# Kernel tuning notes

Measured on AMD Instinct MI355X. Metric: run time of the kernel, lower is better.

## Reference

```python
import jax, jax.numpy as jnp
import numpy as np

K = 5  # kernel_size per dim
# 2^dim = 4 active degree-1 B-spline products per edge (dim=2)
BITS = jnp.array([[0, 0], [1, 0], [0, 1], [1, 1]], dtype=jnp.int32)  # [S,2]


def spline_basis(edge_attr):
    """Open B-spline basis, degree=1, dim=2, kernel_size=5 per dim.
    Returns basis weights [E,S] and flattened kernel indices [E,S]."""
    v = edge_attr * (K - 1)                 # scale pseudo-coords to knot grid
    i0 = jnp.floor(v)
    f = v - i0                              # fractional part, [E,2]
    # per-dim linear weights: f for bit=1, (1-f) for bit=0
    w = jnp.where(BITS[None] == 1, f[:, None, :], 1.0 - f[:, None, :])  # [E,S,2]
    basis = w[..., 0] * w[..., 1]           # [E,S]
    idx = jnp.minimum(i0.astype(jnp.int32)[:, None, :] + BITS[None], K - 1)  # [E,S,2]
    kidx = idx[..., 0] + K * idx[..., 1]    # flatten 2D kernel index -> [0,25)
    return basis, kidx


def spline_conv(x, src, dst, basis, kidx, W, root, bias, n):
    # transform-then-gather: y[n,k,:] = x[n] @ W[k]
    y = jnp.einsum('ni,kio->nko', x, W)                 # [N,25,out]
    g = y[src[:, None], kidx]                           # gather [E,S,out]
    msg = jnp.einsum('es,eso->eo', basis, g)            # weighted sum over S
    agg = jax.ops.segment_sum(msg, dst, num_segments=n)  # scatter-add to targets
    return agg + x @ root + bias                        # root weight + bias


def setup_inputs() -> dict:
    key = jax.random.key(0)
    ks = jax.random.split(key, 8)
    N, E, IN, H, OUT = 50000, 400000, 32, 64, 64
    x = jax.random.normal(ks[0], (N, IN), jnp.float32)
    edge_index = jax.random.randint(ks[1], (2, E), 0, N, dtype=jnp.int32)
    edge_attr = jax.random.uniform(ks[2], (E, 2), jnp.float32)

    def glorot(k, shape):
        fan = shape[-2] + shape[-1]
        return jax.random.normal(k, shape, jnp.float32) * jnp.sqrt(2.0 / fan)

    W1 = glorot(ks[3], (K * K, IN, H));  root1 = glorot(ks[4], (IN, H));  b1 = jnp.zeros((H,), jnp.float32)
    W2 = glorot(ks[5], (K * K, H, OUT)); root2 = glorot(ks[6], (H, OUT)); b2 = jnp.zeros((OUT,), jnp.float32)
    fc_w = glorot(ks[7], (OUT, 3));      fc_b = jnp.zeros((3,), jnp.float32)
    return dict(x=x, edge_index=edge_index, edge_attr=edge_attr,
                W1=W1, root1=root1, b1=b1, W2=W2, root2=root2, b2=b2,
                fc_w=fc_w, fc_b=fc_b)


def reference(x, edge_index, edge_attr, W1, root1, b1, W2, root2, b2, fc_w, fc_b):
    # eval-mode forward (dropout is identity at inference)
    n = x.shape[0]
    src, dst = edge_index[0], edge_index[1]
    basis, kidx = spline_basis(edge_attr)
    h = jax.nn.relu(spline_conv(x, src, dst, basis, kidx, W1, root1, b1, n))
    h = jax.nn.relu(spline_conv(h, src, dst, basis, kidx, W2, root2, b2, n))
    return h @ fc_w + fc_b
```

## Files before the change

kernel.cpp:

```cpp
#include <hip/hip_runtime.h>
#include <stdint.h>

typedef __attribute__((ext_vector_type(8))) short short8;
typedef __attribute__((ext_vector_type(4))) float f32x4;
typedef __attribute__((ext_vector_type(4))) unsigned short ushort4v;

__device__ __forceinline__ unsigned short f2bf(float f) {
    unsigned int u = __float_as_uint(f);
    u = (u + 0x7FFFu + ((u >> 16) & 1u)) >> 16;
    return (unsigned short)u;
}
__device__ __forceinline__ float bf2f(unsigned short h) {
    return __uint_as_float(((unsigned int)h) << 16);
}
__device__ __forceinline__ int cell_of(float ax, float ay) {
    int c0 = (int)floorf(ax * 4.f); c0 = min(max(c0, 0), 3);
    int c1 = (int)floorf(ay * 4.f); c1 = min(max(c1, 0), 3);
    return c0 + 4 * c1;
}

__global__ __launch_bounds__(256) void zero_kernel(int* __restrict__ p, int n) {
    int t = blockIdx.x * 256 + threadIdx.x;
    if (t < n) p[t] = 0;
}

template<int KIN>
__device__ __forceinline__ void pack_cell_elem(const float* __restrict__ W,
                                               unsigned short* __restrict__ pkc, int u) {
    constexpr int KCH = KIN / 8;
    if (u >= 16 * 4 * KCH * 512) return;
    int low9 = u & 511;
    int grp  = u >> 9;
    int kc = grp % KCH; grp /= KCH;
    int c  = grp & 3;
    int cell = grp >> 2;
    int lane = low9 >> 3, j = low9 & 7;
    int k = kc * 32 + (lane >> 4) * 8 + j;
    int t = k / KIN, i = k % KIN;
    int k0 = (cell & 3) + (t & 1);   if (k0 > 4) k0 = 4;
    int k1 = (cell >> 2) + (t >> 1); if (k1 > 4) k1 = 4;
    float val = W[((size_t)(k0 + 5 * k1) * KIN + i) * 64 + (c * 16 + (lane & 15))];
    pkc[u] = f2bf(val);
}

template<int KIN>
__device__ __forceinline__ void pack_root_elem(const float* __restrict__ root,
                                               unsigned short* __restrict__ pkr, int u) {
    constexpr int KCHr = KIN / 32;
    if (u >= 4 * KCHr * 512) return;
    int low9 = u & 511;
    int grp  = u >> 9;
    int lane = low9 >> 3, j = low9 & 7;
    int kc = grp % KCHr, c = grp / KCHr;
    int k = kc * 32 + (lane >> 4) * 8 + j;
    int o = c * 16 + (lane & 15);
    float v = root[(size_t)k * 64 + o];
    unsigned short h = f2bf(v);
    pkr[(size_t)(grp * 2) * 512 + low9]     = h;
    pkr[(size_t)(grp * 2 + 1) * 512 + low9] = f2bf(v - bf2f(h));
}

__global__ __launch_bounds__(256) void prep_kernel(
    const float* __restrict__ attr, const int* __restrict__ dst,
    int* __restrict__ hist, int* __restrict__ dhist, int E,
    const float* __restrict__ W1, const float* __restrict__ W2,
    const float* __restrict__ root1, const float* __restrict__ root2,
    unsigned short* __restrict__ pkc1, unsigned short* __restrict__ pkc2,
    unsigned short* __restrict__ pkr1, unsigned short* __restrict__ pkr2,
    const float* __restrict__ x, unsigned short* __restrict__ xb, int n4,
    int EB)
{
    __shared__ int wcnt[4][16];
    int b = blockIdx.x;
    if (b < EB) {
        int e = b * 256 + threadIdx.x;
        int lane = threadIdx.x & 63, wave = threadIdx.x >> 6;
        int cell = -1;
        if (e < E) {
            float2 a = reinterpret_cast<const float2*>(attr)[e];
            cell = cell_of(a.x, a.y);
            atomicAdd(&dhist[dst[e]], 1);
        }
        #pragma unroll
        for (int c = 0; c < 16; c++) {
            unsigned long long m = __ballot(cell == c);
            if (lane == 0) wcnt[wave][c] = __popcll(m);
        }
        __syncthreads();
        if (threadIdx.x < 16) {
            int c = threadIdx.x;
            int tot = wcnt[0][c] + wcnt[1][c] + wcnt[2][c] + wcnt[3][c];
            if (tot) atomicAdd(&hist[c], tot);
        }
        return;
    }
    b -= EB;
    if (b < 512)  { pack_cell_elem<32>(W1, pkc1, b * 256 + threadIdx.x); return; }
    b -= 512;
    if (b < 1024) { pack_cell_elem<64>(W2, pkc2, b * 256 + threadIdx.x); return; }
    b -= 1024;
    if (b < 8)    { pack_root_elem<32>(root1, pkr1, b * 256 + threadIdx.x); return; }
    b -= 8;
    if (b < 16)   { pack_root_elem<64>(root2, pkr2, b * 256 + threadIdx.x); return; }
    b -= 16;
    {
        int t = b * 256 + threadIdx.x;
        if (t < n4) {
            float4 v = reinterpret_cast<const float4*>(x)[t];
            ushort4v o = { f2bf(v.x), f2bf(v.y), f2bf(v.z), f2bf(v.w) };
            reinterpret_cast<ushort4v*>(xb)[t] = o;
        }
    }
}

__global__ __launch_bounds__(1024) void scanA_kernel(const int* __restrict__ dhist,
                                                     int* __restrict__ nof,
                                                     int* __restrict__ bsum, int Np1) {
    __shared__ int wsum[16];
    int tid = threadIdx.x, lane = tid & 63, w = tid >> 6;
    int i = blockIdx.x * 1024 + tid;
    int v = (i < Np1) ? dhist[i] : 0;
    int s = v;
    #pragma unroll
    for (int off = 1; off < 64; off <<= 1) {
        int t = __shfl_up(s, off);
        if (lane >= off) s += t;
    }
    if (lane == 63) wsum[w] = s;
    __syncthreads();
    if (tid == 0) {
        int a = 0;
        #pragma unroll
        for (int k = 0; k < 16; k++) { int t = wsum[k]; wsum[k] = a; a += t; }
        bsum[blockIdx.x] = a;
    }
    __syncthreads();
    if (i < Np1) nof[i] = wsum[w] + s - v;
}

__global__ void scan_small_kernel(const int* __restrict__ hist, int* __restrict__ off_e,
                                  int* __restrict__ off_b, int* __restrict__ cursor,
                                  const int* __restrict__ bsum, int* __restrict__ bbase, int NB) {
    if (threadIdx.x == 0 && blockIdx.x == 0) {
        int se = 0, sb = 0;
        for (int c = 0; c < 16; c++) {
            off_e[c] = se; off_b[c] = sb; cursor[c] = se;
            se += hist[c]; sb += (hist[c] + 63) >> 6;
        }
        off_e[16] = se; off_b[16] = sb;
        int a = 0;
        for (int bks = 0; bks < NB; bks++) { int t = bsum[bks]; bbase[bks] = a; a += t; }
    }
}

__global__ __launch_bounds__(256) void scatter_kernel(const float* __restrict__ attr,
                                                      const int* __restrict__ src,
                                                      const int* __restrict__ dst,
                                                      const int* __restrict__ nof,
                                                      const int* __restrict__ bbase,
                                                      int4* __restrict__ emeta,
                                                      int* __restrict__ cursor,
                                                      int* __restrict__ dhist, int E) {
    __shared__ int wcnt[4][16];
    __shared__ int wbase[4][16];
    int e = blockIdx.x * 256 + threadIdx.x;
    int lane = threadIdx.x & 63, wave = threadIdx.x >> 6;
    int cell = -1;
    float2 a = {0.f, 0.f};
    int mp = 0, sv = 0;
    if (e < E) {
        a = reinterpret_cast<const float2*>(attr)[e];
        cell = cell_of(a.x, a.y);
        int d = dst[e];
        int rank = atomicSub(&dhist[d], 1) - 1;
        mp = nof[d] + bbase[d >> 10] + rank;
        sv = src[e];
    }
    int myrank = 0;
    #pragma unroll
    for (int c = 0; c < 16; c++) {
        unsigned long long m = __ballot(cell == c);
        if (cell == c) myrank = __popcll(m & ((1ull << lane) - 1ull));
        if (lane == 0) wcnt[wave][c] = __popcll(m);
    }
    __syncthreads();
    if (threadIdx.x < 16) {
        int c = threadIdx.x;
        int t0 = wcnt[0][c], t1 = wcnt[1][c], t2 = wcnt[2][c], t3 = wcnt[3][c];
        int tot = t0 + t1 + t2 + t3;
        int g = tot ? atomicAdd(&cursor[c], tot) : 0;
        wbase[0][c] = g;
        wbase[1][c] = g + t0;
        wbase[2][c] = g + t0 + t1;
        wbase[3][c] = g + t0 + t1 + t2;
    }
    __syncthreads();
    if (e < E) {
        int slot = wbase[wave][cell] + myrank;
        emeta[slot] = make_int4(sv, mp, __float_as_int(a.x), __float_as_int(a.y));
    }
}

template<int KIN>
__global__ __launch_bounds__(256) void layer_kernel(
    const unsigned short* __restrict__ Xb,
    const unsigned short* __restrict__ pkr, float* __restrict__ rt,
    const float* __restrict__ bias, int N, int RG,
    const unsigned short* __restrict__ pkc, unsigned short* __restrict__ msg,
    const int4* __restrict__ emeta,
    const int* __restrict__ off_e, const int* __restrict__ off_b)
{
    constexpr int KCHr = KIN / 32;
    constexpr int KCH  = 4 * KCHr;

    const int lane = threadIdx.x & 63;
    const int wave = threadIdx.x >> 6;
    const int lrow = lane & 15, lch = lane >> 4;

    if (blockIdx.x < RG) {
        const int mbase = blockIdx.x * 64 + wave * 16;
        short8 afrag[KCHr];
        {
            int row = mbase + lrow;
            if (row > N - 1) row = N - 1;
            const unsigned short* ap = Xb + (size_t)row * KIN + lch * 8;
            #pragma unroll
            for (int kc = 0; kc < KCHr; kc++)
                afrag[kc] = *reinterpret_cast<const short8*>(ap + kc * 32);
        }
        f32x4 acc[4];
        #pragma unroll
        for (int c = 0; c < 4; c++) acc[c] = (f32x4){0.f, 0.f, 0.f, 0.f};
        #pragma unroll
        for (int c = 0; c < 4; c++) {
            #pragma unroll
            for (int kc = 0; kc < KCHr; kc++) {
                short8 bh = *reinterpret_cast<const short8*>(pkr + ((size_t)(c * KCHr + kc) * 2    ) * 512 + lane * 8);
                short8 bl = *reinterpret_cast<const short8*>(pkr + ((size_t)(c * KCHr + kc) * 2 + 1) * 512 + lane * 8);
                acc[c] = __builtin_amdgcn_mfma_f32_16x16x32_bf16(afrag[kc], bh, acc[c], 0, 0, 0);
                acc[c] = __builtin_amdgcn_mfma_f32_16x16x32_bf16(afrag[kc], bl, acc[c], 0, 0, 0);
            }
        }
        #pragma unroll
        for (int c = 0; c < 4; c++) {
            int o = c * 16 + lrow;
            float bv = bias[o];
            #pragma unroll
            for (int r = 0; r < 4; r++) {
                int m = mbase + lch * 4 + r;
                if (m < N) rt[(size_t)m * 64 + o] = acc[c][r] + bv;
            }
        }
        return;
    }

    const int b = blockIdx.x - RG;
    if (b >= off_b[16]) return;
    int cell = 0;
    #pragma unroll
    for (int c = 1; c < 16; c++) cell += (b >= off_b[c]);
    const int tile = b - off_b[cell];

    const int ebeg = off_e[cell];
    const int eend = off_e[cell + 1];
    const int eslot = ebeg + (tile * 4 + wave) * 16 + lrow;
    const bool valid = eslot < eend;

    const int4 em = emeta[valid ? eslot : ebeg];
    const int s = em.x;
    const int mp = valid ? em.y : -1;
    const float ax = __int_as_float(em.z);
    const float ay = __int_as_float(em.w);

    const float f0 = ax * 4.f - (float)(cell & 3);
    const float f1 = ay * 4.f - (float)(cell >> 2);
    float w[4] = { (1.f - f0) * (1.f - f1), f0 * (1.f - f1),
                   (1.f - f0) * f1,         f0 * f1 };

    short8 xfrag[KCHr];
    {
        const unsigned short* xp = Xb + (size_t)s * KIN + lch * 8;
        #pragma unroll
        for (int kcr = 0; kcr < KCHr; kcr++)
            xfrag[kcr] = *reinterpret_cast<const short8*>(xp + kcr * 32);
    }

    float wr[4][4];
    int pv[4];
    #pragma unroll
    for (int r = 0; r < 4; r++) {
        int er = lch * 4 + r;
        #pragma unroll
        for (int t = 0; t < 4; t++) wr[t][r] = __shfl(w[t], er);
        pv[r] = __shfl(mp, er);
    }

    const unsigned short* Bp = pkc + (size_t)cell * (4 * KCH * 512) + lane * 8;

    #pragma unroll
    for (int ch = 0; ch < 2; ch++) {
        f32x4 accT[4][2];
        #pragma unroll
        for (int t = 0; t < 4; t++)
            #pragma unroll
            for (int c2 = 0; c2 < 2; c2++)
                accT[t][c2] = (f32x4){0.f, 0.f, 0.f, 0.f};

        #pragma unroll
        for (int t = 0; t < 4; t++) {
            #pragma unroll
            for (int kcr = 0; kcr < KCHr; kcr++) {
                #pragma unroll
                for (int c2 = 0; c2 < 2; c2++) {
                    int c = ch * 2 + c2;
                    short8 bf = *reinterpret_cast<const short8*>(
                        Bp + (size_t)((c * KCH) + (t * KCHr + kcr)) * 512);
                    accT[t][c2] = __builtin_amdgcn_mfma_f32_16x16x32_bf16(xfrag[kcr], bf, accT[t][c2], 0, 0, 0);
                }
            }
        }

        #pragma unroll
        for (int c2 = 0; c2 < 2; c2++) {
            const int o = (ch * 2 + c2) * 16 + lrow;
            #pragma unroll
            for (int r = 0; r < 4; r++) {
                if (pv[r] >= 0) {
                    float m = wr[0][r] * accT[0][c2][r] + wr[1][r] * accT[1][c2][r]
                            + wr[2][r] * accT[2][c2][r] + wr[3][r] * accT[3][c2][r];
                    msg[(size_t)pv[r] * 64 + o] = f2bf(m);
                }
            }
        }
    }
}

template<int MODE>
__global__ __launch_bounds__(256) void segsum_kernel(
    const unsigned short* __restrict__ msg, const float* __restrict__ rt,
    const int* __restrict__ nof, const int* __restrict__ bbase,
    unsigned short* __restrict__ hout,
    const float* __restrict__ fcw, const float* __restrict__ fcb,
    float* __restrict__ out, int N)
{
    int n = blockIdx.x * 4 + (threadIdx.x >> 6);
    if (n >= N) return;
    int lane = threadIdx.x & 63;
    float acc = rt[(size_t)n * 64 + lane];
    int jb = nof[n]     + bbase[n >> 10];
    int je = nof[n + 1] + bbase[(n + 1) >> 10];
    int j = jb;
    for (; j + 3 < je; j += 4) {
        float a0 = bf2f(msg[(size_t)(j + 0) * 64 + lane]);
        float a1 = bf2f(msg[(size_t)(j + 1) * 64 + lane]);
        float a2 = bf2f(msg[(size_t)(j + 2) * 64 + lane]);
        float a3 = bf2f(msg[(size_t)(j + 3) * 64 + lane]);
        acc += a0; acc += a1; acc += a2; acc += a3;
    }
    for (; j < je; j++) acc += bf2f(msg[(size_t)j * 64 + lane]);
    acc = fmaxf(acc, 0.f);
    if (MODE == 0) {
        hout[(size_t)n * 64 + lane] = f2bf(acc);
    } else {
        float p0 = acc * fcw[lane * 3 + 0];
        float p1 = acc * fcw[lane * 3 + 1];
        float p2 = acc * fcw[lane * 3 + 2];
        #pragma unroll
        for (int off = 32; off; off >>= 1) {
            p0 += __shfl_xor(p0, off);
            p1 += __shfl_xor(p1, off);
            p2 += __shfl_xor(p2, off);
        }
        if (lane == 0) {
            out[(size_t)n * 3 + 0] = p0 + fcb[0];
            out[(size_t)n * 3 + 1] = p1 + fcb[1];
            out[(size_t)n * 3 + 2] = p2 + fcb[2];
        }
    }
}

extern "C" void kernel_launch(void* const* d_in, const int* in_sizes, int n_in,
                              void* d_out, int out_size, void* d_ws, size_t ws_size,
                              hipStream_t stream)
{
    const float* x     = (const float*)d_in[0];
    const int*   ei    = (const int*)  d_in[1];
    const float* attr  = (const float*)d_in[2];
    const float* W1    = (const float*)d_in[3];
    const float* root1 = (const float*)d_in[4];
    const float* b1    = (const float*)d_in[5];
    const float* W2    = (const float*)d_in[6];
    const float* root2 = (const float*)d_in[7];
    const float* b2    = (const float*)d_in[8];
    const float* fcw   = (const float*)d_in[9];
    const float* fcb   = (const float*)d_in[10];

    const int N = in_sizes[0] / 32;
    const int E = in_sizes[1] / 2;
    const int* srcp = ei;
    const int* dstp = ei + E;

    char* wsp = (char*)d_ws;
    auto alloc = [&](size_t bytes) -> char* {
        char* p = wsp;
        wsp += (bytes + 255) & ~(size_t)255;
        return p;
    };
    const int NB = (N + 1 + 1023) / 1024;

    float*          rt       = (float*)alloc((size_t)N * 64 * 4);
    unsigned short* xb       = (unsigned short*)alloc((size_t)N * 32 * 2);
    unsigned short* h1b      = (unsigned short*)alloc((size_t)N * 64 * 2);
    unsigned short* pkr1     = (unsigned short*)alloc((size_t)4 * 1 * 2 * 512 * 2);
    unsigned short* pkr2     = (unsigned short*)alloc((size_t)4 * 2 * 2 * 512 * 2);
    unsigned short* pkc1     = (unsigned short*)alloc((size_t)16 * 4 * 4 * 512 * 2);
    unsigned short* pkc2     = (unsigned short*)alloc((size_t)16 * 4 * 8 * 512 * 2);
    int4*           emeta    = (int4*)alloc((size_t)E * 16);
    int*            nof      = (int*)alloc((size_t)(N + 1) * 4);
    int*            bsum     = (int*)alloc((size_t)NB * 4);
    int*            bbase    = (int*)alloc((size_t)NB * 4);
    int*            off_e    = (int*)alloc(17 * 4);
    int*            off_b    = (int*)alloc(17 * 4);
    int*            cursor   = (int*)alloc(16 * 4);
    int*            zbase    = (int*)alloc((size_t)(16 + N + 1) * 4);
    int*            hist     = zbase;
    int*            dhist    = zbase + 16;
    unsigned short* msg      = (unsigned short*)alloc((size_t)E * 64 * 2);

    const int ZN = 16 + N + 1;
    zero_kernel<<<(ZN + 255) / 256, 256, 0, stream>>>(zbase, ZN);

    const int EB = (E + 255) / 256;
    const int CB = (N * 8 + 255) / 256;
    const int prep_grid = EB + 512 + 1024 + 8 + 16 + CB;

    prep_kernel<<<prep_grid, 256, 0, stream>>>(attr, dstp, hist, dhist, E,
                                               W1, W2, root1, root2,
                                               pkc1, pkc2, pkr1, pkr2,
                                               x, xb, N * 8, EB);
    scanA_kernel<<<NB, 1024, 0, stream>>>(dhist, nof, bsum, N + 1);
    scan_small_kernel<<<1, 64, 0, stream>>>(hist, off_e, off_b, cursor, bsum, bbase, NB);
    scatter_kernel<<<EB, 256, 0, stream>>>(attr, srcp, dstp, nof, bbase, emeta, cursor, dhist, E);

    const int RG = (N + 63) / 64;
    const int lgrid = RG + (E + 63) / 64 + 16;
    const int sgrid = (N + 3) / 4;

    layer_kernel<32><<<lgrid, 256, 0, stream>>>(xb, pkr1, rt, b1, N, RG,
                                                pkc1, msg, emeta, off_e, off_b);
    segsum_kernel<0><<<sgrid, 256, 0, stream>>>(msg, rt, nof, bbase, h1b, fcw, fcb, (float*)d_out, N);

    layer_kernel<64><<<lgrid, 256, 0, stream>>>(h1b, pkr2, rt, b2, N, RG,
                                                pkc2, msg, emeta, off_e, off_b);
    segsum_kernel<1><<<sgrid, 256, 0, stream>>>(msg, rt, nof, bbase, nullptr, fcw, fcb, (float*)d_out, N);
}
```

Measured before the change: 192.3 us.

## Stage per-cell spline weights in LDS and process 512-edge chunks per block

```diff
diff --git a/kernel.cpp b/kernel.cpp
--- a/kernel.cpp
+++ b/kernel.cpp
@@ -4,6 +4,8 @@
 typedef __attribute__((ext_vector_type(8))) short short8;
 typedef __attribute__((ext_vector_type(4))) float f32x4;
 typedef __attribute__((ext_vector_type(4))) unsigned short ushort4v;
+
+#define CHUNK 512
 
 __device__ __forceinline__ unsigned short f2bf(float f) {
     unsigned int u = __float_as_uint(f);
@@ -145,7 +147,7 @@
         int se = 0, sb = 0;
         for (int c = 0; c < 16; c++) {
             off_e[c] = se; off_b[c] = sb; cursor[c] = se;
-            se += hist[c]; sb += (hist[c] + 63) >> 6;
+            se += hist[c]; sb += (hist[c] + CHUNK - 1) / CHUNK;
         }
         off_e[16] = se; off_b[16] = sb;
         int a = 0;
@@ -212,6 +214,7 @@
 {
     constexpr int KCHr = KIN / 32;
     constexpr int KCH  = 4 * KCHr;
+    __shared__ unsigned short Blds[4 * KCH * 512];
 
     const int lane = threadIdx.x & 63;
     const int wave = threadIdx.x >> 6;
@@ -259,76 +262,90 @@
     int cell = 0;
     #pragma unroll
     for (int c = 1; c < 16; c++) cell += (b >= off_b[c]);
-    const int tile = b - off_b[cell];
+    const int chunk = b - off_b[cell];
+
+    {
+        const short8* sp = reinterpret_cast<const short8*>(pkc + (size_t)cell * (4 * KCH * 512));
+        short8* dp = reinterpret_cast<short8*>(Blds);
+        #pragma unroll
+        for (int p = 0; p < (4 * KCH * 512 / 8) / 256; p++)
+            dp[p * 256 + threadIdx.x] = sp[p * 256 + threadIdx.x];
+    }
+    __syncthreads();
 
     const int ebeg = off_e[cell];
     const int eend = off_e[cell + 1];
-    const int eslot = ebeg + (tile * 4 + wave) * 16 + lrow;
-    const bool valid = eslot < eend;
-
-    const int4 em = emeta[valid ? eslot : ebeg];
-    const int s = em.x;
-    const int mp = valid ? em.y : -1;
-    const float ax = __int_as_float(em.z);
-    const float ay = __int_as_float(em.w);
-
-    const float f0 = ax * 4.f - (float)(cell & 3);
-    const float f1 = ay * 4.f - (float)(cell >> 2);
-    float w[4] = { (1.f - f0) * (1.f - f1), f0 * (1.f - f1),
-                   (1.f - f0) * f1,         f0 * f1 };
-
-    short8 xfrag[KCHr];
-    {
-        const unsigned short* xp = Xb + (size_t)s * KIN + lch * 8;
-        #pragma unroll
-        for (int kcr = 0; kcr < KCHr; kcr++)
-            xfrag[kcr] = *reinterpret_cast<const short8*>(xp + kcr * 32);
-    }
-
-    float wr[4][4];
-    int pv[4];
-    #pragma unroll
-    for (int r = 0; r < 4; r++) {
-        int er = lch * 4 + r;
-        #pragma unroll
-        for (int t = 0; t < 4; t++) wr[t][r] = __shfl(w[t], er);
-        pv[r] = __shfl(mp, er);
-    }
-
-    const unsigned short* Bp = pkc + (size_t)cell * (4 * KCH * 512) + lane * 8;
-
-    #pragma unroll
-    for (int ch = 0; ch < 2; ch++) {
-        f32x4 accT[4][2];
-        #pragma unroll
-        for (int t = 0; t < 4; t++)
-            #pragma unroll
-            for (int c2 = 0; c2 < 2; c2++)
-                accT[t][c2] = (f32x4){0.f, 0.f, 0.f, 0.f};
-
-        #pragma unroll
-        for (int t = 0; t < 4; t++) {
-            #pragma unroll
-            for (int kcr = 0; kcr < KCHr; kcr++) {
+    const int base = ebeg + chunk * CHUNK;
+    const float c0f = (float)(cell & 3), c1f = (float)(cell >> 2);
+
+    for (int tt = 0; tt < 8; tt++) {
+        const int tbase = base + (tt * 4 + wave) * 16;
+        if (tbase >= eend) continue;
+        const int eslot = tbase + lrow;
+        const bool valid = eslot < eend;
+
+        const int4 em = emeta[valid ? eslot : ebeg];
+        const int s  = em.x;
+        const int mp = valid ? em.y : -1;
+        const float ax = __int_as_float(em.z);
+        const float ay = __int_as_float(em.w);
+
+        const float f0 = ax * 4.f - c0f;
+        const float f1 = ay * 4.f - c1f;
+        float w[4] = { (1.f - f0) * (1.f - f1), f0 * (1.f - f1),
+                       (1.f - f0) * f1,         f0 * f1 };
+
+        short8 xfrag[KCHr];
+        {
+            const unsigned short* xp = Xb + (size_t)s * KIN + lch * 8;
+            #pragma unroll
+            for (int kcr = 0; kcr < KCHr; kcr++)
+                xfrag[kcr] = *reinterpret_cast<const short8*>(xp + kcr * 32);
+        }
+
+        float wr[4][4];
+        int pv[4];
+        #pragma unroll
+        for (int r = 0; r < 4; r++) {
+            int er = lch * 4 + r;
+            #pragma unroll
+            for (int t = 0; t < 4; t++) wr[t][r] = __shfl(w[t], er);
+            pv[r] = __shfl(mp, er);
+        }
+
+        #pragma unroll
+        for (int ch = 0; ch < 2; ch++) {
+            f32x4 accT[4][2];
+            #pragma unroll
+            for (int t = 0; t < 4; t++)
                 #pragma unroll
-                for (int c2 = 0; c2 < 2; c2++) {
-                    int c = ch * 2 + c2;
-                    short8 bf = *reinterpret_cast<const short8*>(
-                        Bp + (size_t)((c * KCH) + (t * KCHr + kcr)) * 512);
-                    accT[t][c2] = __builtin_amdgcn_mfma_f32_16x16x32_bf16(xfrag[kcr], bf, accT[t][c2], 0, 0, 0);
+                for (int c2 = 0; c2 < 2; c2++)
+                    accT[t][c2] = (f32x4){0.f, 0.f, 0.f, 0.f};
+
+            #pragma unroll
+            for (int t = 0; t < 4; t++) {
+                #pragma unroll
+                for (int kcr = 0; kcr < KCHr; kcr++) {
+                    #pragma unroll
+                    for (int c2 = 0; c2 < 2; c2++) {
+                        int c = ch * 2 + c2;
+                        short8 bf = *reinterpret_cast<const short8*>(
+                            &Blds[(size_t)((c * KCH) + (t * KCHr + kcr)) * 512 + lane * 8]);
+                        accT[t][c2] = __builtin_amdgcn_mfma_f32_16x16x32_bf16(xfrag[kcr], bf, accT[t][c2], 0, 0, 0);
+                    }
                 }
             }
-        }
-
-        #pragma unroll
-        for (int c2 = 0; c2 < 2; c2++) {
-            const int o = (ch * 2 + c2) * 16 + lrow;
-            #pragma unroll
-            for (int r = 0; r < 4; r++) {
-                if (pv[r] >= 0) {
-                    float m = wr[0][r] * accT[0][c2][r] + wr[1][r] * accT[1][c2][r]
-                            + wr[2][r] * accT[2][c2][r] + wr[3][r] * accT[3][c2][r];
-                    msg[(size_t)pv[r] * 64 + o] = f2bf(m);
+
+            #pragma unroll
+            for (int c2 = 0; c2 < 2; c2++) {
+                const int o = (ch * 2 + c2) * 16 + lrow;
+                #pragma unroll
+                for (int r = 0; r < 4; r++) {
+                    if (pv[r] >= 0) {
+                        float m = wr[0][r] * accT[0][c2][r] + wr[1][r] * accT[1][c2][r]
+                                + wr[2][r] * accT[2][c2][r] + wr[3][r] * accT[3][c2][r];
+                        msg[(size_t)pv[r] * 64 + o] = f2bf(m);
+                    }
                 }
             }
         }
@@ -443,7 +460,7 @@
     scatter_kernel<<<EB, 256, 0, stream>>>(attr, srcp, dstp, nof, bbase, emeta, cursor, dhist, E);
 
     const int RG = (N + 63) / 64;
-    const int lgrid = RG + (E + 63) / 64 + 16;
+    const int lgrid = RG + (E + CHUNK - 1) / CHUNK + 16;
     const int sgrid = (N + 3) / 4;
 
     layer_kernel<32><<<lgrid, 256, 0, stream>>>(xb, pkr1, rt, b1, N, RG,
```

New measurement: 181.4 us. 5.7% less time.
